# Optimization experiments

Measured on AMD Instinct MI355X. Metric: run time of the kernel, lower is better.

Reference implementation:

```python
import jax, jax.numpy as jnp
import numpy as np

DIM = 768
HEADS = 12
DH = DIM // HEADS
SCALE = DH ** -0.5


def setup_inputs() -> dict:
    key = jax.random.key(0)
    ks = jax.random.split(key, 8)
    B, N = 8, 1024
    x = jax.random.normal(ks[0], (B, N, DIM), dtype=jnp.float32)
    rpb = jax.random.normal(ks[1], (1, HEADS, N, N), dtype=jnp.float32)
    s = DIM ** -0.5
    W_qkv = jax.random.normal(ks[2], (DIM, 3 * DIM), dtype=jnp.float32) * s
    W_out = jax.random.normal(ks[3], (DIM, DIM), dtype=jnp.float32) * s
    b_out = jnp.zeros((DIM,), dtype=jnp.float32)
    ln_g = jnp.ones((DIM,), dtype=jnp.float32)
    ln_b = jnp.zeros((DIM,), dtype=jnp.float32)
    return {"x": x, "relative_position_bias": rpb, "W_qkv": W_qkv,
            "W_out": W_out, "b_out": b_out, "ln_g": ln_g, "ln_b": ln_b}


def reference(x, relative_position_bias, W_qkv, W_out, b_out, ln_g, ln_b):
    # LayerNorm (eps matches torch default 1e-5)
    mu = jnp.mean(x, axis=-1, keepdims=True)
    var = jnp.mean(jnp.square(x - mu), axis=-1, keepdims=True)
    xn = (x - mu) * jax.lax.rsqrt(var + 1e-5) * ln_g + ln_b

    qkv = xn @ W_qkv                                  # [b,n,3*dim]
    q, k, v = jnp.split(qkv, 3, axis=-1)
    B, N, _ = x.shape
    reshape = lambda t: t.reshape(B, N, HEADS, DH).transpose(0, 2, 1, 3)  # b h n d
    q, k, v = reshape(q), reshape(k), reshape(v)

    scores = jnp.einsum('bhid,bhjd->bhij', q, k) * SCALE + relative_position_bias
    attn = jax.nn.softmax(scores, axis=-1)            # dropout p=0.0 -> identity
    out = jnp.einsum('bhij,bhjd->bhid', attn, v)
    out = out.transpose(0, 2, 1, 3).reshape(B, N, HEADS * DH)
    return out @ W_out + b_out
```

## Files before the change

kernel.cpp:

```cpp
#include <hip/hip_runtime.h>
#include <hip/hip_bf16.h>
#include <math.h>

#define BATCH 8
#define NSEQ  1024
#define DIMM  768
#define NHEAD 12
#define DHEAD 64
#define SCALE 0.125f
#define ROWS  (BATCH * NSEQ)

typedef __hip_bfloat16 bf16;
typedef __bf16 bf16x8 __attribute__((ext_vector_type(8)));
typedef float  f32x4  __attribute__((ext_vector_type(4)));

#if __has_builtin(__builtin_amdgcn_global_load_lds)
#define HAVE_GLL 1
typedef __attribute__((address_space(3))) void lds_void_t;
typedef const __attribute__((address_space(1))) void gbl_void_t;
__device__ __forceinline__ void gload16(const void* g, void* l) {
    __builtin_amdgcn_global_load_lds((gbl_void_t*)g, (lds_void_t*)l, 16, 0, 0);
}
#else
#define HAVE_GLL 0
#endif

__device__ __forceinline__ unsigned pk2(float a, float b) {
    union { unsigned u; bf16 h[2]; } x;
    x.h[0] = __float2bfloat16(a);
    x.h[1] = __float2bfloat16(b);
    return x.u;
}

#define NT_QKV (DIMM / 32 * (3 * DIMM) / 32)
#define NT_OUT (DIMM / 32 * DIMM / 32)

__device__ __forceinline__ void transpose_tile(const float* __restrict__ W,
                                               bf16* __restrict__ Wt,
                                               int K, int N, int n0, int k0,
                                               int tx, int ty, float (*t)[33]) {
#pragma unroll
    for (int i = 0; i < 32; i += 8)
        t[ty + i][tx] = W[(size_t)(k0 + ty + i) * N + n0 + tx];
    __syncthreads();
#pragma unroll
    for (int i = 0; i < 32; i += 8)
        Wt[(size_t)(n0 + ty + i) * K + k0 + tx] = __float2bfloat16(t[tx][ty + i]);
}

__global__ __launch_bounds__(256) void prep_kernel(const float* __restrict__ x,
                                                   const float* __restrict__ g,
                                                   const float* __restrict__ bta,
                                                   bf16* __restrict__ y,
                                                   const float* __restrict__ Wq,
                                                   bf16* __restrict__ WqT,
                                                   const float* __restrict__ Wo,
                                                   bf16* __restrict__ WoT) {
    __shared__ float ps[4], pq[4];
    __shared__ float mean_s, rstd_s;
    __shared__ float t[32][33];
    int bid = blockIdx.x;
    int tid = threadIdx.x;

    if (bid < ROWS) {
        const float* xr = x + (size_t)bid * DIMM;
        float v[3];
        float s = 0.f, sq = 0.f;
#pragma unroll
        for (int i = 0; i < 3; ++i) {
            v[i] = xr[tid + 256 * i];
            s += v[i];
            sq += v[i] * v[i];
        }
#pragma unroll
        for (int off = 32; off >= 1; off >>= 1) {
            s  += __shfl_down(s, off);
            sq += __shfl_down(sq, off);
        }
        int wid = tid >> 6, lane = tid & 63;
        if (lane == 0) { ps[wid] = s; pq[wid] = sq; }
        __syncthreads();
        if (tid == 0) {
            float S = ps[0] + ps[1] + ps[2] + ps[3];
            float Q = pq[0] + pq[1] + pq[2] + pq[3];
            float mean = S * (1.0f / DIMM);
            float var  = Q * (1.0f / DIMM) - mean * mean;
            mean_s = mean;
            rstd_s = rsqrtf(fmaxf(var, 0.f) + 1e-5f);
        }
        __syncthreads();
        float mean = mean_s, rstd = rstd_s;
        bf16* yr = y + (size_t)bid * DIMM;
#pragma unroll
        for (int i = 0; i < 3; ++i) {
            int c = tid + 256 * i;
            yr[c] = __float2bfloat16((v[i] - mean) * rstd * g[c] + bta[c]);
        }
    } else if (bid < ROWS + NT_QKV) {
        int idx = bid - ROWS;
        int tx = tid & 31, ty = tid >> 5;
        int n0 = (idx % (3 * DIMM / 32)) * 32;
        int k0 = (idx / (3 * DIMM / 32)) * 32;
        transpose_tile(Wq, WqT, DIMM, 3 * DIMM, n0, k0, tx, ty, t);
    } else {
        int idx = bid - ROWS - NT_QKV;
        int tx = tid & 31, ty = tid >> 5;
        int n0 = (idx % (DIMM / 32)) * 32;
        int k0 = (idx / (DIMM / 32)) * 32;
        transpose_tile(Wo, WoT, DIMM, DIMM, n0, k0, tx, ty, t);
    }
}

template <bool OUT_BF16>
__global__ __launch_bounds__(256) void gemm_mfma(const bf16* __restrict__ A,
                                                 const bf16* __restrict__ Bt,
                                                 const float* __restrict__ bias,
                                                 void* __restrict__ Cv,
                                                 int M, int Nn, int K) {
    __shared__ bf16 As[2][128][32];
    __shared__ bf16 Bs[2][128][32];
    int tid = threadIdx.x;
    int wave = tid >> 6, lane = tid & 63, quad = lane >> 4, l16 = lane & 15;
    int wm = (wave >> 1) * 64, wn = (wave & 1) * 64;
    int m0 = blockIdx.y * 128, n0 = blockIdx.x * 128;

    f32x4 acc[4][4] = {};

#if HAVE_GLL
    const char* Ag = (const char*)(A  + (size_t)(m0 + (tid >> 2)) * K + (tid & 3) * 8);
    const char* Bg = (const char*)(Bt + (size_t)(n0 + (tid >> 2)) * K + (tid & 3) * 8);
    char* AsB = (char*)&As[0][0][0] + tid * 16;
    char* BsB = (char*)&Bs[0][0][0] + tid * 16;
    const size_t radv = (size_t)64 * K * 2;

    gload16(Ag, AsB);
    gload16(Ag + radv, AsB + 4096);
    gload16(Bg, BsB);
    gload16(Bg + radv, BsB + 4096);
    Ag += 64; Bg += 64;
    __syncthreads();

    int cur = 0;
    for (int k0 = 0; k0 < K; k0 += 32) {
        int nxt = cur ^ 1;
        if (k0 + 32 < K) {
            gload16(Ag, AsB + nxt * 8192);
            gload16(Ag + radv, AsB + nxt * 8192 + 4096);
            gload16(Bg, BsB + nxt * 8192);
            gload16(Bg + radv, BsB + nxt * 8192 + 4096);
            Ag += 64; Bg += 64;
        }
#else
    int srow = tid >> 1;
    int sk = (tid & 1) * 16;
    const bf16* Ap = A  + (size_t)(m0 + srow) * K + sk;
    const bf16* Bp = Bt + (size_t)(n0 + srow) * K + sk;
    {
        uint4 a0 = *(const uint4*)(Ap);
        uint4 a1 = *(const uint4*)(Ap + 8);
        uint4 b0 = *(const uint4*)(Bp);
        uint4 b1 = *(const uint4*)(Bp + 8);
        *(uint4*)&As[0][srow][sk]     = a0;
        *(uint4*)&As[0][srow][sk + 8] = a1;
        *(uint4*)&Bs[0][srow][sk]     = b0;
        *(uint4*)&Bs[0][srow][sk + 8] = b1;
    }
    __syncthreads();
    int cur = 0;
    for (int k0 = 0; k0 < K; k0 += 32) {
        int nxt = cur ^ 1;
        uint4 a0, a1, b0, b1;
        if (k0 + 32 < K) {
            a0 = *(const uint4*)(Ap + k0 + 32);
            a1 = *(const uint4*)(Ap + k0 + 40);
            b0 = *(const uint4*)(Bp + k0 + 32);
            b1 = *(const uint4*)(Bp + k0 + 40);
        }
#endif
        bf16x8 af[4], bf_[4];
#pragma unroll
        for (int i = 0; i < 4; ++i) {
            af[i]  = *(const bf16x8*)&As[cur][wm + i * 16 + l16][quad * 8];
            bf_[i] = *(const bf16x8*)&Bs[cur][wn + i * 16 + l16][quad * 8];
        }
#pragma unroll
        for (int mi = 0; mi < 4; ++mi)
#pragma unroll
            for (int ni = 0; ni < 4; ++ni)
                acc[mi][ni] = __builtin_amdgcn_mfma_f32_16x16x32_bf16(
                    af[mi], bf_[ni], acc[mi][ni], 0, 0, 0);
#if !HAVE_GLL
        if (k0 + 32 < K) {
            *(uint4*)&As[nxt][srow][sk]     = a0;
            *(uint4*)&As[nxt][srow][sk + 8] = a1;
            *(uint4*)&Bs[nxt][srow][sk]     = b0;
            *(uint4*)&Bs[nxt][srow][sk + 8] = b1;
        }
#endif
        __syncthreads();
        cur = nxt;
    }

    float bv[4] = {0.f, 0.f, 0.f, 0.f};
    if (!OUT_BF16 && bias) {
#pragma unroll
        for (int ni = 0; ni < 4; ++ni) bv[ni] = bias[n0 + wn + ni * 16 + l16];
    }
#pragma unroll
    for (int mi = 0; mi < 4; ++mi)
#pragma unroll
        for (int reg = 0; reg < 4; ++reg) {
            size_t row = m0 + wm + mi * 16 + quad * 4 + reg;
#pragma unroll
            for (int ni = 0; ni < 4; ++ni) {
                int col = n0 + wn + ni * 16 + l16;
                float val = acc[mi][ni][reg] + bv[ni];
                if (OUT_BF16)
                    ((bf16*)Cv)[row * Nn + col] = __float2bfloat16(val);
                else
                    ((float*)Cv)[row * Nn + col] = val;
            }
        }
}

#define KTILEB (64 * 3 * DIMM * 2)
#define NBLK   (BATCH * NHEAD * (NSEQ / 64))

__global__ __launch_bounds__(256, 4) void attn_mfma(const bf16* __restrict__ qkv,
                                                    const float* __restrict__ rpb,
                                                    bf16* __restrict__ outb) {
    __shared__ char KsRaw[2][8192];
    __shared__ unsigned Vt32[2][64][36];
    __shared__ bf16 Ps[4][16][72];

    int tid = threadIdx.x;
    int wave = tid >> 6, lane = tid & 63, quad = lane >> 4, l16 = lane & 15;

    int p   = blockIdx.x;
    int wid = (p & 7) * (NBLK / 8) + (p >> 3);
    int h   = wid >> 7;
    int rem = wid & 127;
    int b   = rem >> 4;
    int mt  = rem & 15;
    int m0  = mt * 64;

    const bf16* qrow = qkv + (size_t)(b * NSEQ + m0 + wave * 16 + l16) * (3 * DIMM) + h * DHEAD;
    bf16x8 qf0 = *(const bf16x8*)(qrow + quad * 8);
    bf16x8 qf1 = *(const bf16x8*)(qrow + 32 + quad * 8);

    const float* rp = rpb + ((size_t)h * NSEQ + (m0 + wave * 16 + l16)) * NSEQ;

#if HAVE_GLL
    const char* kgl = (const char*)(qkv + (size_t)(b * NSEQ + wave * 16 + l16) * (3 * DIMM)
                                    + DIMM + h * DHEAD + quad * 8);
    char* kdst = &KsRaw[0][0] + tid * 16 + wave * 1024;
#else
    int ksr = tid >> 2, ksd = (tid & 3) * 16;
    const bf16* kgf = qkv + (size_t)(b * NSEQ + ksr) * (3 * DIMM) + DIMM + h * DHEAD + ksd;
#endif

    int vk = (tid >> 3) * 2;
    int vd = (tid & 7) * 8;
    int vkp = tid >> 3;
    const bf16* vg = qkv + (size_t)(b * NSEQ + vk) * (3 * DIMM) + 2 * DIMM + h * DHEAD + vd;
    int wblk = (((vkp >> 2) ^ (vd >> 3)) << 2) | (vkp & 3);

    float m_s = -INFINITY, l_s = 0.f;
    f32x4 acco[4] = {};

#if HAVE_GLL
    gload16(kgl, kdst);
    gload16(kgl + 64, kdst + 1024);
#endif
    uint4 va = *(const uint4*)(vg);
    uint4 vb = *(const uint4*)(vg + 3 * DIMM);
#if !HAVE_GLL
    {
        uint4 k0v = *(const uint4*)(kgf);
        uint4 k1v = *(const uint4*)(kgf + 8);
        char* d0 = &KsRaw[0][0] + (ksr >> 4) * 2048 + (ksd >> 5) * 1024 + ((((ksd >> 3) & 3) * 16 + (ksr & 15)) * 16);
        *(uint4*)d0 = k0v;
        char* d1 = &KsRaw[0][0] + (ksr >> 4) * 2048 + ((ksd + 8) >> 5) * 1024 + (((((ksd + 8) >> 3) & 3) * 16 + (ksr & 15)) * 16);
        *(uint4*)d1 = k1v;
    }
#endif
    {
        union { uint4 q; unsigned short u[8]; } A_, B_;
        A_.q = va; B_.q = vb;
#pragma unroll
        for (int j = 0; j < 8; ++j)
            Vt32[0][vd + j][wblk] = (unsigned)A_.u[j] | ((unsigned)B_.u[j] << 16);
    }
    float4 rv[4];
#pragma unroll
    for (int t = 0; t < 4; ++t)
        rv[t] = *(const float4*)&rp[t * 16 + quad * 4];
    __syncthreads();

    for (int kt = 0; kt < 16; ++kt) {
        int cur = kt & 1, nxt = cur ^ 1;

        float4 rvn[4];
        if (kt + 1 < 16) {
#if HAVE_GLL
            const char* kg2 = kgl + (size_t)(kt + 1) * KTILEB;
            gload16(kg2, kdst + nxt * 8192);
            gload16(kg2 + 64, kdst + nxt * 8192 + 1024);
#endif
            const bf16* v2 = vg + (size_t)(kt + 1) * 64 * (3 * DIMM);
            va = *(const uint4*)(v2);
            vb = *(const uint4*)(v2 + 3 * DIMM);
            const float* rpn = rp + (kt + 1) * 64;
#pragma unroll
            for (int t = 0; t < 4; ++t)
                rvn[t] = *(const float4*)&rpn[t * 16 + quad * 4];
        }

        f32x4 accs[4] = {};
        __builtin_amdgcn_s_setprio(1);
#pragma unroll
        for (int t = 0; t < 4; ++t) {
            const char* kb = &KsRaw[cur][0] + t * 2048 + (quad * 16 + l16) * 16;
            bf16x8 kf0 = *(const bf16x8*)(kb);
            bf16x8 kf1 = *(const bf16x8*)(kb + 1024);
            accs[t] = __builtin_amdgcn_mfma_f32_16x16x32_bf16(kf0, qf0, accs[t], 0, 0, 0);
            accs[t] = __builtin_amdgcn_mfma_f32_16x16x32_bf16(kf1, qf1, accs[t], 0, 0, 0);
        }
        __builtin_amdgcn_s_setprio(0);

        float mx = -INFINITY;
        {
            float rb[4][4] = {{rv[0].x, rv[0].y, rv[0].z, rv[0].w},
                              {rv[1].x, rv[1].y, rv[1].z, rv[1].w},
                              {rv[2].x, rv[2].y, rv[2].z, rv[2].w},
                              {rv[3].x, rv[3].y, rv[3].z, rv[3].w}};
#pragma unroll
            for (int t = 0; t < 4; ++t)
#pragma unroll
                for (int r = 0; r < 4; ++r) {
                    accs[t][r] = fmaf(accs[t][r], SCALE, rb[t][r]);
                    mx = fmaxf(mx, accs[t][r]);
                }
        }
        mx = fmaxf(mx, __shfl_xor(mx, 16));
        mx = fmaxf(mx, __shfl_xor(mx, 32));

        if (__any(mx > m_s + 8.0f)) {
            float mn = fmaxf(m_s, mx);
            float alpha = __expf(m_s - mn);
            m_s = mn;
            l_s *= alpha;
            float ab[4];
#pragma unroll
            for (int r = 0; r < 4; ++r) ab[r] = __shfl(alpha, quad * 4 + r);
#pragma unroll
            for (int dt = 0; dt < 4; ++dt)
#pragma unroll
                for (int r = 0; r < 4; ++r) acco[dt][r] *= ab[r];
        }

        float sum = 0.f;
#pragma unroll
        for (int t = 0; t < 4; ++t)
#pragma unroll
            for (int r = 0; r < 4; ++r) {
                float pv = __expf(accs[t][r] - m_s);
                accs[t][r] = pv;
                sum += pv;
            }
        sum += __shfl_xor(sum, 16);
        sum += __shfl_xor(sum, 32);
        l_s += sum;

#pragma unroll
        for (int t = 0; t < 4; ++t) {
            uint2 w;
            w.x = pk2(accs[t][0], accs[t][1]);
            w.y = pk2(accs[t][2], accs[t][3]);
            *(uint2*)&Ps[wave][l16][t * 16 + quad * 4] = w;
        }
        __asm__ volatile("s_waitcnt lgkmcnt(0)" ::: "memory");

        __builtin_amdgcn_s_setprio(1);
#pragma unroll
        for (int s = 0; s < 2; ++s) {
            bf16x8 pf = *(const bf16x8*)&Ps[wave][l16][s * 32 + quad * 8];
#pragma unroll
            for (int dt = 0; dt < 4; ++dt) {
                int row = dt * 16 + l16;
                int sblk = (((s * 4 + quad) ^ ((row >> 3) & 7)) << 2);
                bf16x8 vf = *(const bf16x8*)&Vt32[cur][row][sblk];
                acco[dt] = __builtin_amdgcn_mfma_f32_16x16x32_bf16(pf, vf, acco[dt], 0, 0, 0);
            }
        }
        __builtin_amdgcn_s_setprio(0);

        if (kt + 1 < 16) {
            union { uint4 q; unsigned short u[8]; } A_, B_;
            A_.q = va; B_.q = vb;
#pragma unroll
            for (int j = 0; j < 8; ++j)
                Vt32[nxt][vd + j][wblk] = (unsigned)A_.u[j] | ((unsigned)B_.u[j] << 16);
#pragma unroll
            for (int t = 0; t < 4; ++t) rv[t] = rvn[t];
        }
        __syncthreads();
    }

    float invl[4];
#pragma unroll
    for (int r = 0; r < 4; ++r) invl[r] = 1.f / __shfl(l_s, quad * 4 + r);
    bf16* orow = outb + (size_t)(b * NSEQ + m0 + wave * 16) * DIMM + h * DHEAD;
#pragma unroll
    for (int dt = 0; dt < 4; ++dt)
#pragma unroll
        for (int r = 0; r < 4; ++r)
            orow[(size_t)(quad * 4 + r) * DIMM + dt * 16 + l16] =
                __float2bfloat16(acco[dt][r] * invl[r]);
}

extern "C" void kernel_launch(void* const* d_in, const int* in_sizes, int n_in,
                              void* d_out, int out_size, void* d_ws, size_t ws_size,
                              hipStream_t stream) {
    const float* x     = (const float*)d_in[0];
    const float* rpb   = (const float*)d_in[1];
    const float* W_qkv = (const float*)d_in[2];
    const float* W_out = (const float*)d_in[3];
    const float* b_out = (const float*)d_in[4];
    const float* ln_g  = (const float*)d_in[5];
    const float* ln_b  = (const float*)d_in[6];
    float* out = (float*)d_out;

    char* p = (char*)d_ws;
    bf16* xn    = (bf16*)p; p += (size_t)ROWS * DIMM * 2;
    bf16* qkv   = (bf16*)p; p += (size_t)ROWS * 3 * DIMM * 2;
    bf16* attn  = (bf16*)p; p += (size_t)ROWS * DIMM * 2;
    bf16* WqkvT = (bf16*)p; p += (size_t)3 * DIMM * DIMM * 2;
    bf16* WoutT = (bf16*)p; p += (size_t)DIMM * DIMM * 2;

    prep_kernel<<<ROWS + NT_QKV + NT_OUT, 256, 0, stream>>>(
        x, ln_g, ln_b, xn, W_qkv, WqkvT, W_out, WoutT);

    gemm_mfma<true><<<dim3(3 * DIMM / 128, ROWS / 128), 256, 0, stream>>>(
        xn, WqkvT, nullptr, qkv, ROWS, 3 * DIMM, DIMM);

    attn_mfma<<<NBLK, 256, 0, stream>>>(qkv, rpb, attn);

    gemm_mfma<false><<<dim3(DIMM / 128, ROWS / 128), 256, 0, stream>>>(
        attn, WoutT, b_out, out, ROWS, DIMM, DIMM);
}
```

Measured before the change: 266.0 us.

## Process two 64-row query tiles per attention block to reuse K/V tiles

Each attention block now handles 128 query rows, with every wave owning two 16-row query slices (A and B) that share the same K and V tiles loaded into LDS. This halves the K/V global traffic and LDS staging per query row and gives each wave twice the MFMA work per load. In exchange register pressure roughly doubles, launch bounds drop to 3 waves-per-SIMD occupancy hint, and the grid halves. The relative-position-bias loads are no longer prefetched one iteration ahead but issued at the top of each iteration.

Result: faster. 260.4 us (-2.1%).

```diff
diff --git a/kernel.cpp b/kernel.cpp
--- a/kernel.cpp
+++ b/kernel.cpp
@@ -224,31 +224,35 @@
 }
 
 #define KTILEB (64 * 3 * DIMM * 2)
-#define NBLK   (BATCH * NHEAD * (NSEQ / 64))
-
-__global__ __launch_bounds__(256, 4) void attn_mfma(const bf16* __restrict__ qkv,
+#define NBLK   (BATCH * NHEAD * (NSEQ / 128))
+
+__global__ __launch_bounds__(256, 3) void attn_mfma(const bf16* __restrict__ qkv,
                                                     const float* __restrict__ rpb,
                                                     bf16* __restrict__ outb) {
     __shared__ char KsRaw[2][8192];
     __shared__ unsigned Vt32[2][64][36];
-    __shared__ bf16 Ps[4][16][72];
+    __shared__ bf16 Ps[4][2][16][72];
 
     int tid = threadIdx.x;
     int wave = tid >> 6, lane = tid & 63, quad = lane >> 4, l16 = lane & 15;
 
     int p   = blockIdx.x;
     int wid = (p & 7) * (NBLK / 8) + (p >> 3);
-    int h   = wid >> 7;
-    int rem = wid & 127;
-    int b   = rem >> 4;
-    int mt  = rem & 15;
-    int m0  = mt * 64;
-
-    const bf16* qrow = qkv + (size_t)(b * NSEQ + m0 + wave * 16 + l16) * (3 * DIMM) + h * DHEAD;
-    bf16x8 qf0 = *(const bf16x8*)(qrow + quad * 8);
-    bf16x8 qf1 = *(const bf16x8*)(qrow + 32 + quad * 8);
-
-    const float* rp = rpb + ((size_t)h * NSEQ + (m0 + wave * 16 + l16)) * NSEQ;
+    int h   = wid >> 6;
+    int rem = wid & 63;
+    int b   = rem >> 3;
+    int mt  = rem & 7;
+    int m0  = mt * 128;
+
+    const bf16* qrowA = qkv + (size_t)(b * NSEQ + m0 + wave * 16 + l16) * (3 * DIMM) + h * DHEAD;
+    const bf16* qrowB = qrowA + (size_t)64 * (3 * DIMM);
+    bf16x8 qfA0 = *(const bf16x8*)(qrowA + quad * 8);
+    bf16x8 qfA1 = *(const bf16x8*)(qrowA + 32 + quad * 8);
+    bf16x8 qfB0 = *(const bf16x8*)(qrowB + quad * 8);
+    bf16x8 qfB1 = *(const bf16x8*)(qrowB + 32 + quad * 8);
+
+    const float* rpA = rpb + ((size_t)h * NSEQ + (m0 + wave * 16 + l16)) * NSEQ;
+    const float* rpB = rpA + (size_t)64 * NSEQ;
 
 #if HAVE_GLL
     const char* kgl = (const char*)(qkv + (size_t)(b * NSEQ + wave * 16 + l16) * (3 * DIMM)
@@ -265,8 +269,9 @@
     const bf16* vg = qkv + (size_t)(b * NSEQ + vk) * (3 * DIMM) + 2 * DIMM + h * DHEAD + vd;
     int wblk = (((vkp >> 2) ^ (vd >> 3)) << 2) | (vkp & 3);
 
-    float m_s = -INFINITY, l_s = 0.f;
-    f32x4 acco[4] = {};
+    float mA = -INFINITY, lA = 0.f;
+    float mB = -INFINITY, lB = 0.f;
+    f32x4 accoA[4] = {}, accoB[4] = {};
 
 #if HAVE_GLL
     gload16(kgl, kdst);
@@ -291,16 +296,22 @@
         for (int j = 0; j < 8; ++j)
             Vt32[0][vd + j][wblk] = (unsigned)A_.u[j] | ((unsigned)B_.u[j] << 16);
     }
-    float4 rv[4];
-#pragma unroll
-    for (int t = 0; t < 4; ++t)
-        rv[t] = *(const float4*)&rp[t * 16 + quad * 4];
     __syncthreads();
 
     for (int kt = 0; kt < 16; ++kt) {
         int cur = kt & 1, nxt = cur ^ 1;
 
-        float4 rvn[4];
+        float4 rvA[4], rvB[4];
+        {
+            const float* rka = rpA + kt * 64;
+            const float* rkb = rpB + kt * 64;
+#pragma unroll
+            for (int t = 0; t < 4; ++t) {
+                rvA[t] = *(const float4*)&rka[t * 16 + quad * 4];
+                rvB[t] = *(const float4*)&rkb[t * 16 + quad * 4];
+            }
+        }
+
         if (kt + 1 < 16) {
 #if HAVE_GLL
             const char* kg2 = kgl + (size_t)(kt + 1) * KTILEB;
@@ -310,87 +321,117 @@
             const bf16* v2 = vg + (size_t)(kt + 1) * 64 * (3 * DIMM);
             va = *(const uint4*)(v2);
             vb = *(const uint4*)(v2 + 3 * DIMM);
-            const float* rpn = rp + (kt + 1) * 64;
-#pragma unroll
-            for (int t = 0; t < 4; ++t)
-                rvn[t] = *(const float4*)&rpn[t * 16 + quad * 4];
-        }
-
-        f32x4 accs[4] = {};
+        }
+
+        f32x4 accsA[4] = {}, accsB[4] = {};
         __builtin_amdgcn_s_setprio(1);
 #pragma unroll
         for (int t = 0; t < 4; ++t) {
             const char* kb = &KsRaw[cur][0] + t * 2048 + (quad * 16 + l16) * 16;
             bf16x8 kf0 = *(const bf16x8*)(kb);
             bf16x8 kf1 = *(const bf16x8*)(kb + 1024);
-            accs[t] = __builtin_amdgcn_mfma_f32_16x16x32_bf16(kf0, qf0, accs[t], 0, 0, 0);
-            accs[t] = __builtin_amdgcn_mfma_f32_16x16x32_bf16(kf1, qf1, accs[t], 0, 0, 0);
+            accsA[t] = __builtin_amdgcn_mfma_f32_16x16x32_bf16(kf0, qfA0, accsA[t], 0, 0, 0);
+            accsA[t] = __builtin_amdgcn_mfma_f32_16x16x32_bf16(kf1, qfA1, accsA[t], 0, 0, 0);
+            accsB[t] = __builtin_amdgcn_mfma_f32_16x16x32_bf16(kf0, qfB0, accsB[t], 0, 0, 0);
+            accsB[t] = __builtin_amdgcn_mfma_f32_16x16x32_bf16(kf1, qfB1, accsB[t], 0, 0, 0);
         }
         __builtin_amdgcn_s_setprio(0);
 
-        float mx = -INFINITY;
+        float mxA = -INFINITY, mxB = -INFINITY;
         {
-            float rb[4][4] = {{rv[0].x, rv[0].y, rv[0].z, rv[0].w},
-                              {rv[1].x, rv[1].y, rv[1].z, rv[1].w},
-                              {rv[2].x, rv[2].y, rv[2].z, rv[2].w},
-                              {rv[3].x, rv[3].y, rv[3].z, rv[3].w}};
+            float rbA[4][4] = {{rvA[0].x, rvA[0].y, rvA[0].z, rvA[0].w},
+                               {rvA[1].x, rvA[1].y, rvA[1].z, rvA[1].w},
+                               {rvA[2].x, rvA[2].y, rvA[2].z, rvA[2].w},
+                               {rvA[3].x, rvA[3].y, rvA[3].z, rvA[3].w}};
+            float rbB[4][4] = {{rvB[0].x, rvB[0].y, rvB[0].z, rvB[0].w},
+                               {rvB[1].x, rvB[1].y, rvB[1].z, rvB[1].w},
+                               {rvB[2].x, rvB[2].y, rvB[2].z, rvB[2].w},
+                               {rvB[3].x, rvB[3].y, rvB[3].z, rvB[3].w}};
 #pragma unroll
             for (int t = 0; t < 4; ++t)
 #pragma unroll
                 for (int r = 0; r < 4; ++r) {
-                    accs[t][r] = fmaf(accs[t][r], SCALE, rb[t][r]);
-                    mx = fmaxf(mx, accs[t][r]);
+                    accsA[t][r] = fmaf(accsA[t][r], SCALE, rbA[t][r]);
+                    mxA = fmaxf(mxA, accsA[t][r]);
+                    accsB[t][r] = fmaf(accsB[t][r], SCALE, rbB[t][r]);
+                    mxB = fmaxf(mxB, accsB[t][r]);
                 }
         }
-        mx = fmaxf(mx, __shfl_xor(mx, 16));
-        mx = fmaxf(mx, __shfl_xor(mx, 32));
-
-        if (__any(mx > m_s + 8.0f)) {
-            float mn = fmaxf(m_s, mx);
-            float alpha = __expf(m_s - mn);
-            m_s = mn;
-            l_s *= alpha;
+        mxA = fmaxf(mxA, __shfl_xor(mxA, 16));
+        mxA = fmaxf(mxA, __shfl_xor(mxA, 32));
+        mxB = fmaxf(mxB, __shfl_xor(mxB, 16));
+        mxB = fmaxf(mxB, __shfl_xor(mxB, 32));
+
+        if (__any(mxA > mA + 8.0f)) {
+            float mn = fmaxf(mA, mxA);
+            float alpha = __expf(mA - mn);
+            mA = mn;
+            lA *= alpha;
             float ab[4];
 #pragma unroll
             for (int r = 0; r < 4; ++r) ab[r] = __shfl(alpha, quad * 4 + r);
 #pragma unroll
             for (int dt = 0; dt < 4; ++dt)
 #pragma unroll
-                for (int r = 0; r < 4; ++r) acco[dt][r] *= ab[r];
-        }
-
-        float sum = 0.f;
+                for (int r = 0; r < 4; ++r) accoA[dt][r] *= ab[r];
+        }
+        if (__any(mxB > mB + 8.0f)) {
+            float mn = fmaxf(mB, mxB);
+            float alpha = __expf(mB - mn);
+            mB = mn;
+            lB *= alpha;
+            float ab[4];
+#pragma unroll
+            for (int r = 0; r < 4; ++r) ab[r] = __shfl(alpha, quad * 4 + r);
+#pragma unroll
+            for (int dt = 0; dt < 4; ++dt)
+#pragma unroll
+                for (int r = 0; r < 4; ++r) accoB[dt][r] *= ab[r];
+        }
+
+        float sumA = 0.f, sumB = 0.f;
 #pragma unroll
         for (int t = 0; t < 4; ++t)
 #pragma unroll
             for (int r = 0; r < 4; ++r) {
-                float pv = __expf(accs[t][r] - m_s);
-                accs[t][r] = pv;
-                sum += pv;
+                float pa = __expf(accsA[t][r] - mA);
+                accsA[t][r] = pa;
+                sumA += pa;
+                float pb = __expf(accsB[t][r] - mB);
+                accsB[t][r] = pb;
+                sumB += pb;
             }
-        sum += __shfl_xor(sum, 16);
-        sum += __shfl_xor(sum, 32);
-        l_s += sum;
+        sumA += __shfl_xor(sumA, 16);
+        sumA += __shfl_xor(sumA, 32);
+        sumB += __shfl_xor(sumB, 16);
+        sumB += __shfl_xor(sumB, 32);
+        lA += sumA;
+        lB += sumB;
 
 #pragma unroll
         for (int t = 0; t < 4; ++t) {
-            uint2 w;
-            w.x = pk2(accs[t][0], accs[t][1]);
-            w.y = pk2(accs[t][2], accs[t][3]);
-            *(uint2*)&Ps[wave][l16][t * 16 + quad * 4] = w;
+            uint2 wA, wB;
+            wA.x = pk2(accsA[t][0], accsA[t][1]);
+            wA.y = pk2(accsA[t][2], accsA[t][3]);
+            wB.x = pk2(accsB[t][0], accsB[t][1]);
+            wB.y = pk2(accsB[t][2], accsB[t][3]);
+            *(uint2*)&Ps[wave][0][l16][t * 16 + quad * 4] = wA;
+            *(uint2*)&Ps[wave][1][l16][t * 16 + quad * 4] = wB;
         }
         __asm__ volatile("s_waitcnt lgkmcnt(0)" ::: "memory");
 
         __builtin_amdgcn_s_setprio(1);
 #pragma unroll
         for (int s = 0; s < 2; ++s) {
-            bf16x8 pf = *(const bf16x8*)&Ps[wave][l16][s * 32 + quad * 8];
+            bf16x8 pfA = *(const bf16x8*)&Ps[wave][0][l16][s * 32 + quad * 8];
+            bf16x8 pfB = *(const bf16x8*)&Ps[wave][1][l16][s * 32 + quad * 8];
 #pragma unroll
             for (int dt = 0; dt < 4; ++dt) {
                 int row = dt * 16 + l16;
                 int sblk = (((s * 4 + quad) ^ ((row >> 3) & 7)) << 2);
                 bf16x8 vf = *(const bf16x8*)&Vt32[cur][row][sblk];
-                acco[dt] = __builtin_amdgcn_mfma_f32_16x16x32_bf16(pf, vf, acco[dt], 0, 0, 0);
+                accoA[dt] = __builtin_amdgcn_mfma_f32_16x16x32_bf16(pfA, vf, accoA[dt], 0, 0, 0);
+                accoB[dt] = __builtin_amdgcn_mfma_f32_16x16x32_bf16(pfB, vf, accoB[dt], 0, 0, 0);
             }
         }
         __builtin_amdgcn_s_setprio(0);
@@ -401,22 +442,27 @@
 #pragma unroll
             for (int j = 0; j < 8; ++j)
                 Vt32[nxt][vd + j][wblk] = (unsigned)A_.u[j] | ((unsigned)B_.u[j] << 16);
-#pragma unroll
-            for (int t = 0; t < 4; ++t) rv[t] = rvn[t];
         }
         __syncthreads();
     }
 
-    float invl[4];
-#pragma unroll
-    for (int r = 0; r < 4; ++r) invl[r] = 1.f / __shfl(l_s, quad * 4 + r);
-    bf16* orow = outb + (size_t)(b * NSEQ + m0 + wave * 16) * DIMM + h * DHEAD;
+    float invlA[4], invlB[4];
+#pragma unroll
+    for (int r = 0; r < 4; ++r) {
+        invlA[r] = 1.f / __shfl(lA, quad * 4 + r);
+        invlB[r] = 1.f / __shfl(lB, quad * 4 + r);
+    }
+    bf16* orowA = outb + (size_t)(b * NSEQ + m0 + wave * 16) * DIMM + h * DHEAD;
+    bf16* orowB = orowA + (size_t)64 * DIMM;
 #pragma unroll
     for (int dt = 0; dt < 4; ++dt)
 #pragma unroll
-        for (int r = 0; r < 4; ++r)
-            orow[(size_t)(quad * 4 + r) * DIMM + dt * 16 + l16] =
-                __float2bfloat16(acco[dt][r] * invl[r]);
+        for (int r = 0; r < 4; ++r) {
+            orowA[(size_t)(quad * 4 + r) * DIMM + dt * 16 + l16] =
+                __float2bfloat16(accoA[dt][r] * invlA[r]);
+            orowB[(size_t)(quad * 4 + r) * DIMM + dt * 16 + l16] =
+                __float2bfloat16(accoB[dt][r] * invlB[r]);
+        }
 }
 
 extern "C" void kernel_launch(void* const* d_in, const int* in_sizes, int n_in,
```
